# Performance work log

Hardware: AMD Instinct MI355X
Metric: run time of the kernel (lower is better)

## Reference

```python
import jax, jax.numpy as jnp
import numpy as np

N_NODES = 50000
N_EDGES = 800000
N_GRAPHS = 64
IN_DIM = 128
HID = 256
N_LAYERS = 4
N_PROT = 5
N_CLASSES = 1
EPS = 1e-12


def setup_inputs() -> dict:
    key = jax.random.key(0)
    ks = jax.random.split(key, 10)
    h = jax.random.normal(ks[0], (N_NODES, IN_DIM), jnp.float32)
    src = jax.random.randint(ks[1], (N_EDGES,), 0, N_NODES, dtype=jnp.int32)
    dst = jax.random.randint(ks[2], (N_EDGES,), 0, N_NODES, dtype=jnp.int32)
    graph_id = jnp.sort(jax.random.randint(ks[3], (N_NODES,), 0, N_GRAPHS, dtype=jnp.int32))
    W_emb = jax.random.normal(ks[4], (IN_DIM, HID), jnp.float32) * 0.05
    b_emb = jnp.zeros((HID,), jnp.float32)
    Ws = jax.random.normal(ks[5], (N_LAYERS, 2 * HID, HID), jnp.float32) * 0.05
    bs = jnp.zeros((N_LAYERS, HID), jnp.float32)
    p_pos = jax.random.uniform(ks[6], (N_PROT, HID), jnp.float32)
    p_neg = jax.random.uniform(ks[7], (N_PROT, HID), jnp.float32)
    W_fc = jax.random.normal(ks[8], (N_CLASSES, 2 * N_PROT), jnp.float32) * 0.1
    return dict(h=h, src=src, dst=dst, graph_id=graph_id, W_emb=W_emb,
                b_emb=b_emb, Ws=Ws, bs=bs, p_pos=p_pos, p_neg=p_neg, W_fc=W_fc)


def _segment_mean(x, seg, num):
    # sum over segments, divide by count (empty segments -> 0, like DGL mean)
    s = jax.ops.segment_sum(x, seg, num_segments=num)
    cnt = jax.ops.segment_sum(jnp.ones((x.shape[0],), x.dtype), seg, num_segments=num)
    return s / jnp.maximum(cnt, 1.0)[:, None]


def _forward(h, src, dst, graph_id, W_emb, b_emb, Ws, bs, p_pos, p_neg, W_fc):
    x = h @ W_emb + b_emb  # [N, HID]
    for l in range(N_LAYERS):
        # mean aggregation of neighbor messages (copy_src -> mean at dst)
        c = _segment_mean(x[src], dst, N_NODES)  # [N, HID]
        bundle = jnp.concatenate([x, c], axis=1) @ Ws[l] + bs[l]  # [N, HID]
        # F.normalize(p=2, dim=1) then relu activation, then residual add
        norm = jnp.linalg.norm(bundle, axis=1, keepdims=True)
        bundle = bundle / jnp.maximum(norm, EPS)
        x = x + jax.nn.relu(bundle)
    hg = _segment_mean(x, graph_id, N_GRAPHS)  # dgl.mean_nodes -> [G, HID]

    def sims(P):
        d = jnp.sum((hg[:, None, :] - P[None, :, :]) ** 2, axis=-1)  # [G, P]
        return jnp.log((d + 1.0) / (d + EPS))

    ss = jnp.concatenate([sims(p_pos), sims(p_neg)], axis=1)  # [G, 2P]
    y = ss @ W_fc.T  # [G, n_classes]
    return jax.nn.sigmoid(y).squeeze()


def reference(h, src, dst, graph_id, W_emb, b_emb, Ws, bs, p_pos, p_neg, W_fc):
    return _forward(h, src, dst, graph_id, W_emb, b_emb, Ws, bs, p_pos, p_neg, W_fc)
```

## Files before the change

### kernel.cpp

```cpp
#include <hip/hip_runtime.h>
#include <math.h>

#define N_NODESC 50000
#define NPAD 50048
#define N_EDGESC 800000
#define N_GRAPHSC 64
#define IN_DIMC 128
#define HIDC 256
#define N_LAYERSC 4
#define EPSV 1e-12f

#define NBUCK 196
#define EPB 4096
#define NBLK1 196
#define WCONV_BLKS 2176

typedef __attribute__((ext_vector_type(8))) short short8;
typedef __attribute__((ext_vector_type(4))) float floatx4;
typedef __attribute__((ext_vector_type(2))) float floatx2;

__device__ __forceinline__ unsigned short f2b(float f) {
    union { float f; unsigned u; } v; v.f = f;
    unsigned r = v.u + 0x7FFFu + ((v.u >> 16) & 1u);
    return (unsigned short)(r >> 16);
}
__device__ __forceinline__ unsigned pkb(float a, float b) {
    return (unsigned)f2b(a) | ((unsigned)f2b(b) << 16);
}
__device__ __forceinline__ unsigned char f2q(float v) {
    return (unsigned char)(__builtin_amdgcn_cvt_pk_fp8_f32(v, v, 0, false) & 0xFF);
}
__device__ __forceinline__ float q2f(unsigned u) {
    floatx2 t = __builtin_amdgcn_cvt_pk_f32_fp8(u, false);
    return t.x;
}
__device__ __forceinline__ unsigned pk4q(float a, float b, float c, float d) {
    unsigned lo = (unsigned)__builtin_amdgcn_cvt_pk_fp8_f32(a, b, 0, false) & 0xFFFFu;
    unsigned hi = (unsigned)__builtin_amdgcn_cvt_pk_fp8_f32(c, d, 0, false) << 16;
    return lo | hi;
}
__device__ __forceinline__ void ldscp16(const void* g, void* l) {
    __builtin_amdgcn_global_load_lds(
        (const __attribute__((address_space(1))) unsigned int*)g,
        (__attribute__((address_space(3))) unsigned int*)l, 16, 0, 0);
}

__global__ __launch_bounds__(256) void k_pre1(const float* __restrict__ Wemb,
        const float* __restrict__ Ws, unsigned short* __restrict__ wsw,
        unsigned char* __restrict__ wq, const int* __restrict__ gid,
        int* __restrict__ gstart, const int* __restrict__ dst,
        int* __restrict__ gbcnt) {
    __shared__ int bc[256];
    int b = blockIdx.x;
    int t = threadIdx.x;
    if (b < WCONV_BLKS) {
        int idx = b * 256 + t;
        const int EMB = IN_DIMC * HIDC;
        const int LYR = 2 * HIDC * HIDC;
        if (idx < EMB) {
            int k = idx >> 8, n = idx & 255;
            int off = (((k >> 5) * 16 + (n >> 4)) * 64 + ((((k >> 3) & 3) << 4) | (n & 15))) * 8 + (k & 7);
            wsw[off] = f2b(Wemb[idx]);
        } else if (idx < EMB + N_LAYERSC * LYR) {
            int r = idx - EMB;
            int l = r >> 17;
            int r2 = r & (LYR - 1);
            int k = r2 >> 8, n = r2 & 255;
            int off = (((k >> 5) * 16 + (n >> 4)) * 64 + ((((k >> 3) & 3) << 4) | (n & 15))) * 8 + (k & 7);
            wq[(size_t)l * LYR + off] = f2q(Ws[r]);
        }
    } else if (b == WCONV_BLKS) {
        int g = t;
        if (g <= N_GRAPHSC) {
            int lo = 0, hi = N_NODESC;
            while (lo < hi) {
                int mid = (lo + hi) >> 1;
                if (gid[mid] < g) lo = mid + 1; else hi = mid;
            }
            gstart[g] = lo;
        }
    } else {
        bc[t] = 0;
        __syncthreads();
        int e0 = (b - WCONV_BLKS - 1) * EPB;
        for (int i = t; i < EPB; i += 256) {
            int e = e0 + i;
            if (e < N_EDGESC) atomicAdd(&bc[dst[e] >> 8], 1);
        }
        __syncthreads();
        if (t < NBUCK && bc[t] > 0) atomicAdd(&gbcnt[t], bc[t]);
    }
}

__global__ __launch_bounds__(256) void k_bscan(const int* __restrict__ gbcnt,
        int* __restrict__ boffB, int* __restrict__ gcurB) {
    __shared__ int s[256];
    int t = threadIdx.x;
    int v = (t < NBUCK) ? gbcnt[t] : 0;
    s[t] = v;
    __syncthreads();
    for (int d = 1; d < 256; d <<= 1) {
        int u = (t >= d) ? s[t - d] : 0;
        __syncthreads();
        s[t] += u;
        __syncthreads();
    }
    if (t < NBUCK) {
        int excl = s[t] - v;
        boffB[t] = excl;
        gcurB[t] = excl;
    }
    if (t == 0) boffB[NBUCK] = N_EDGESC;
}

__global__ __launch_bounds__(256, 4) void k_scat_egemm(const int* __restrict__ src,
        const int* __restrict__ dst, int* __restrict__ gcurB,
        unsigned* __restrict__ ebpack, const float* __restrict__ h,
        const unsigned short* __restrict__ wsw, const float* __restrict__ bias,
        unsigned char* __restrict__ xq) {
    __shared__ int bc[256];
    __shared__ int cur[256];
    if (blockIdx.x < NBLK1) {
        int t = threadIdx.x;
        bc[t] = 0;
        __syncthreads();
        int e0 = blockIdx.x * EPB;
        for (int i = t; i < EPB; i += 256) {
            int e = e0 + i;
            if (e < N_EDGESC) atomicAdd(&bc[dst[e] >> 8], 1);
        }
        __syncthreads();
        if (t < NBUCK)
            cur[t] = (bc[t] > 0) ? atomicAdd(&gcurB[t], bc[t]) : 0;
        __syncthreads();
        for (int i = t; i < EPB; i += 256) {
            int e = e0 + i;
            if (e < N_EDGESC) {
                int d = dst[e];
                int b = d >> 8;
                int pos = atomicAdd(&cur[b], 1);
                ebpack[pos] = (unsigned)src[e] | ((unsigned)(d & 255) << 16);
            }
        }
        return;
    }
    int tid = threadIdx.x;
    int wn = tid >> 6;
    int lane = tid & 63;
    int quad = lane >> 4;
    int l15 = lane & 15;
    int row0 = (blockIdx.x - NBLK1) * 32;

    floatx4 acc[2][4];
    #pragma unroll
    for (int mt = 0; mt < 2; mt++)
        #pragma unroll
        for (int n = 0; n < 4; n++)
            acc[mt][n] = (floatx4){0.f, 0.f, 0.f, 0.f};

    int r0 = row0 + l15;
    int r1 = row0 + 16 + l15;
    bool ok0 = r0 < N_NODESC, ok1 = r1 < N_NODESC;
    const float* h0 = h + (size_t)r0 * IN_DIMC + quad * 8;
    const float* h1 = h + (size_t)r1 * IN_DIMC + quad * 8;
    const unsigned short* bp = wsw + ((size_t)(wn * 4) * 64 + lane) * 8;

    #pragma unroll
    for (int ks = 0; ks < 4; ks++) {
        float4 f00 = ok0 ? *(const float4*)(h0 + ks * 32)     : (float4){0,0,0,0};
        float4 f01 = ok0 ? *(const float4*)(h0 + ks * 32 + 4) : (float4){0,0,0,0};
        float4 f10 = ok1 ? *(const float4*)(h1 + ks * 32)     : (float4){0,0,0,0};
        float4 f11 = ok1 ? *(const float4*)(h1 + ks * 32 + 4) : (float4){0,0,0,0};
        short8 afr[2], bfr[4];
        uint4 av;
        av.x = pkb(f00.x, f00.y); av.y = pkb(f00.z, f00.w);
        av.z = pkb(f01.x, f01.y); av.w = pkb(f01.z, f01.w);
        afr[0] = *(short8*)&av;
        av.x = pkb(f10.x, f10.y); av.y = pkb(f10.z, f10.w);
        av.z = pkb(f11.x, f11.y); av.w = pkb(f11.z, f11.w);
        afr[1] = *(short8*)&av;
        const unsigned short* wp = bp + (size_t)ks * 8192;
        #pragma unroll
        for (int n = 0; n < 4; n++)
            bfr[n] = *(const short8*)(wp + n * 512);
        #pragma unroll
        for (int mt = 0; mt < 2; mt++)
            #pragma unroll
            for (int n = 0; n < 4; n++)
                acc[mt][n] = __builtin_amdgcn_mfma_f32_16x16x32_bf16(
                    afr[mt], bfr[n], acc[mt][n], 0, 0, 0);
    }

    float bv[4];
    #pragma unroll
    for (int n = 0; n < 4; n++) bv[n] = bias[wn * 64 + n * 16 + l15];
    #pragma unroll
    for (int mt = 0; mt < 2; mt++) {
        #pragma unroll
        for (int r = 0; r < 4; r++) {
            int row = row0 + mt * 16 + quad * 4 + r;
            if (row < N_NODESC) {
                #pragma unroll
                for (int n = 0; n < 4; n++) {
                    int col = wn * 64 + n * 16 + l15;
                    float v = acc[mt][n][r] + bv[n];
                    xq[(size_t)row * HIDC + col] = f2q(v);
                }
            }
        }
    }
}

__global__ __launch_bounds__(256) void k_bbuild(const unsigned* __restrict__ ebpack,
        const int* __restrict__ boffB, int* __restrict__ offs,
        unsigned short* __restrict__ esrc) {
    __shared__ int deg[256];
    __shared__ int lofs[256];
    __shared__ unsigned short img[12288];
    int b = blockIdx.x;
    int t = threadIdx.x;
    int bbase = boffB[b];
    int cnt = boffB[b + 1] - bbase;
    deg[t] = 0;
    __syncthreads();
    for (int i = t; i < cnt; i += 256)
        atomicAdd(&deg[ebpack[bbase + i] >> 16], 1);
    __syncthreads();
    int v = deg[t];
    lofs[t] = v;
    __syncthreads();
    for (int d = 1; d < 256; d <<= 1) {
        int u = (t >= d) ? lofs[t - d] : 0;
        __syncthreads();
        lofs[t] += u;
        __syncthreads();
    }
    int excl = lofs[t] - v;
    int node = b * 256 + t;
    if (node < N_NODESC) offs[node] = bbase + excl;
    if (b == NBUCK - 1 && t == 0) offs[N_NODESC] = N_EDGESC;
    deg[t] = excl;
    __syncthreads();
    for (int i = t; i < cnt; i += 256) {
        unsigned p = ebpack[bbase + i];
        int pos = atomicAdd(&deg[p >> 16], 1);
        img[pos] = (unsigned short)(p & 0xFFFF);
    }
    __syncthreads();
    for (int i = t; i < cnt; i += 256)
        esrc[bbase + i] = img[i];
}

__global__ __launch_bounds__(256, 8) void k_aggregate(const unsigned char* __restrict__ xq,
        const int* __restrict__ offs, const unsigned short* __restrict__ esrc,
        unsigned char* __restrict__ cq) {
    int gidx = blockIdx.x * 256 + threadIdx.x;
    int node = gidx >> 5;
    int lane = threadIdx.x & 31;
    if (node >= N_NODESC) return;
    int beg = offs[node], end = offs[node + 1];
    float a[8];
    #pragma unroll
    for (int j = 0; j < 8; j++) a[j] = 0.f;
    size_t loff = (size_t)lane * 8;
    int e = beg;
    #define ACC8(v) do { \
        floatx2 t0 = __builtin_amdgcn_cvt_pk_f32_fp8((v).x, false); \
        floatx2 t1 = __builtin_amdgcn_cvt_pk_f32_fp8((v).x, true);  \
        floatx2 t2 = __builtin_amdgcn_cvt_pk_f32_fp8((v).y, false); \
        floatx2 t3 = __builtin_amdgcn_cvt_pk_f32_fp8((v).y, true);  \
        a[0] += t0.x; a[1] += t0.y; a[2] += t1.x; a[3] += t1.y;     \
        a[4] += t2.x; a[5] += t2.y; a[6] += t3.x; a[7] += t3.y;     \
    } while (0)
    for (; e + 8 <= end; e += 8) {
        int sidx[8];
        #pragma unroll
        for (int j = 0; j < 8; j++) sidx[j] = esrc[e + j];
        uint2 v[8];
        #pragma unroll
        for (int j = 0; j < 8; j++)
            v[j] = *(const uint2*)(xq + (size_t)sidx[j] * HIDC + loff);
        #pragma unroll
        for (int j = 0; j < 8; j++) ACC8(v[j]);
    }
    if (e + 4 <= end) {
        int sidx[4];
        #pragma unroll
        for (int j = 0; j < 4; j++) sidx[j] = esrc[e + j];
        uint2 v[4];
        #pragma unroll
        for (int j = 0; j < 4; j++)
            v[j] = *(const uint2*)(xq + (size_t)sidx[j] * HIDC + loff);
        #pragma unroll
        for (int j = 0; j < 4; j++) ACC8(v[j]);
        e += 4;
    }
    for (; e < end; e++) {
        uint2 v = *(const uint2*)(xq + (size_t)esrc[e] * HIDC + loff);
        ACC8(v);
    }
    #undef ACC8
    float w = 1.0f / (float)max(end - beg, 1);
    uint2 o;
    o.x = pk4q(a[0] * w, a[1] * w, a[2] * w, a[3] * w);
    o.y = pk4q(a[4] * w, a[5] * w, a[6] * w, a[7] * w);
    *(uint2*)(cq + (size_t)node * HIDC + loff) = o;
}

template<bool LAST>
__global__ __launch_bounds__(256, 6) void k_lgemm(unsigned char* __restrict__ xq,
        const unsigned char* __restrict__ cq, const unsigned char* __restrict__ wq,
        const float* __restrict__ bias, const int* __restrict__ gid,
        float* __restrict__ hg) {
    __shared__ unsigned long long panelA64[1024];
    __shared__ unsigned long long panelC64[1024];
    __shared__ float rs[32];
    __shared__ signed char ggl[LAST ? 32 : 1];
    __shared__ int g0s;
    unsigned char* panelA = (unsigned char*)panelA64;
    unsigned char* panelC = (unsigned char*)panelC64;
    int tid = threadIdx.x;
    int w = tid >> 6;
    int lane = tid & 63;
    int quad = lane >> 4;
    int l15 = lane & 15;
    int row0 = blockIdx.x * 32;

    {
        int sboff = w * 2048 + lane * 16;
        #pragma unroll
        for (int i = 0; i < 2; i++) {
            int ldsoff = sboff + i * 1024;
            int r = ldsoff >> 8;
            int ch = (ldsoff & 255) >> 4;
            int lc = ch ^ (r & 15);
            ldscp16(xq + (size_t)(row0 + r) * HIDC + lc * 16, &panelA[w * 2048 + i * 1024]);
            ldscp16(cq + (size_t)(row0 + r) * HIDC + lc * 16, &panelC[w * 2048 + i * 1024]);
        }
    }
    __syncthreads();

    floatx4 acc[2][4];
    #pragma unroll
    for (int mt = 0; mt < 2; mt++)
        #pragma unroll
        for (int n = 0; n < 4; n++)
            acc[mt][n] = (floatx4){0.f, 0.f, 0.f, 0.f};

    const unsigned char* bp = wq + ((size_t)(w * 4) * 64 + lane) * 8;

    long long bcur[4], bnxt[4], acur[2], anxt[2];
    #pragma unroll
    for (int n = 0; n < 4; n++) bcur[n] = *(const long long*)(bp + n * 512);
    #pragma unroll
    for (int mt = 0; mt < 2; mt++) {
        int row = mt * 16 + l15;
        int lc = quad >> 1;
        int phys = lc ^ (row & 15);
        acur[mt] = *(const long long*)&panelA[row * 256 + phys * 16 + (quad & 1) * 8];
    }

    #pragma unroll
    for (int st = 0; st < 16; st++) {
        if (st < 15) {
            const unsigned char* wp = bp + (size_t)(st + 1) * 8192;
            #pragma unroll
            for (int n = 0; n < 4; n++)
                bnxt[n] = *(const long long*)(wp + n * 512);
            const unsigned char* pan2 = (st + 1 < 8) ? panelA : panelC;
            int ks2 = (st + 1) & 7;
            #pragma unroll
            for (int mt = 0; mt < 2; mt++) {
                int row = mt * 16 + l15;
                int lc = ks2 * 2 + (quad >> 1);
                int phys = lc ^ (row & 15);
                anxt[mt] = *(const long long*)&pan2[row * 256 + phys * 16 + (quad & 1) * 8];
            }
        }
        #pragma unroll
        for (int mt = 0; mt < 2; mt++)
            #pragma unroll
            for (int n = 0; n < 4; n++)
                acc[mt][n] = __builtin_amdgcn_mfma_f32_16x16x32_fp8_fp8(
                    acur[mt], bcur[n], acc[mt][n], 0, 0, 0);
        #pragma unroll
        for (int n = 0; n < 4; n++) bcur[n] = bnxt[n];
        #pragma unroll
        for (int mt = 0; mt < 2; mt++) acur[mt] = anxt[mt];
    }

    float bv[4];
    #pragma unroll
    for (int n = 0; n < 4; n++) bv[n] = bias[w * 64 + n * 16 + l15];
    #pragma unroll
    for (int mt = 0; mt < 2; mt++)
        #pragma unroll
        for (int n = 0; n < 4; n++)
            #pragma unroll
            for (int r = 0; r < 4; r++)
                acc[mt][n][r] += bv[n];

    __syncthreads();
    if (tid < 32) rs[tid] = 0.f;
    if constexpr (LAST) {
        if (tid < 32) {
            int g0 = gid[min(row0, N_NODESC - 1)];
            int gv = gid[min(row0 + tid, N_NODESC - 1)] - g0;
            ggl[tid] = (signed char)min(gv, 3);
            if (tid == 0) g0s = g0;
        }
    }
    __syncthreads();
    #pragma unroll
    for (int mt = 0; mt < 2; mt++) {
        #pragma unroll
        for (int r = 0; r < 4; r++) {
            float p = acc[mt][0][r] * acc[mt][0][r] + acc[mt][1][r] * acc[mt][1][r]
                    + acc[mt][2][r] * acc[mt][2][r] + acc[mt][3][r] * acc[mt][3][r];
            p += __shfl_xor(p, 1);
            p += __shfl_xor(p, 2);
            p += __shfl_xor(p, 4);
            p += __shfl_xor(p, 8);
            if (l15 == 0) atomicAdd(&rs[mt * 16 + quad * 4 + r], p);
        }
    }
    __syncthreads();

    #pragma unroll
    for (int mt = 0; mt < 2; mt++) {
        #pragma unroll
        for (int r = 0; r < 4; r++) {
            int lrow = mt * 16 + quad * 4 + r;
            int row = row0 + lrow;
            float inv = 1.0f / fmaxf(sqrtf(rs[mt * 16 + quad * 4 + r]), EPSV);
            #pragma unroll
            for (int n = 0; n < 4; n++) {
                int phys = (w * 4 + n) ^ (lrow & 15);
                float xo = q2f((unsigned)panelA[lrow * 256 + phys * 16 + l15]);
                float nv = xo + fmaxf(acc[mt][n][r] * inv, 0.f);
                if constexpr (LAST) {
                    acc[mt][n][r] = nv;
                } else if (row < N_NODESC) {
                    int col = w * 64 + n * 16 + l15;
                    xq[(size_t)row * HIDC + col] = f2q(nv);
                }
            }
        }
    }
    if constexpr (LAST) {
        int nspan = (int)ggl[31] + 1;
        int g0 = g0s;
        for (int gl = 0; gl < nspan; gl++) {
            float s[4] = {0.f, 0.f, 0.f, 0.f};
            #pragma unroll
            for (int mt = 0; mt < 2; mt++) {
                #pragma unroll
                for (int r = 0; r < 4; r++) {
                    int lrow = mt * 16 + quad * 4 + r;
                    bool m = ((int)ggl[lrow] == gl) && (row0 + lrow < N_NODESC);
                    float f = m ? 1.f : 0.f;
                    #pragma unroll
                    for (int n = 0; n < 4; n++) s[n] += f * acc[mt][n][r];
                }
            }
            #pragma unroll
            for (int n = 0; n < 4; n++) {
                s[n] += __shfl_xor(s[n], 16);
                s[n] += __shfl_xor(s[n], 32);
            }
            if (quad == 0) {
                #pragma unroll
                for (int n = 0; n < 4; n++)
                    atomicAdd(&hg[(g0 + gl) * HIDC + w * 64 + n * 16 + l15], s[n]);
            }
        }
    }
}

__global__ __launch_bounds__(256) void k_readout(const float* __restrict__ hg,
        const int* __restrict__ gstart, const float* __restrict__ ppos,
        const float* __restrict__ pneg, const float* __restrict__ wfc,
        float* __restrict__ out) {
    __shared__ float red[256];
    __shared__ float ss[10];
    int t = threadIdx.x;
    int g = blockIdx.x;
    int beg = gstart[g], end = gstart[g + 1];
    float inv = 1.0f / (float)max(end - beg, 1);
    float hgv = hg[g * HIDC + t] * inv;
    for (int p = 0; p < 10; p++) {
        const float* P = (p < 5) ? (ppos + p * HIDC) : (pneg + (p - 5) * HIDC);
        float d = hgv - P[t];
        red[t] = d * d;
        __syncthreads();
        for (int s2 = 128; s2 > 0; s2 >>= 1) {
            if (t < s2) red[t] += red[t + s2];
            __syncthreads();
        }
        if (t == 0) {
            float dd = red[0];
            ss[p] = logf((dd + 1.0f) / (dd + EPSV));
        }
        __syncthreads();
    }
    if (t == 0) {
        float y = 0.f;
        #pragma unroll
        for (int p = 0; p < 10; p++) y += ss[p] * wfc[p];
        out[g] = 1.0f / (1.0f + expf(-y));
    }
}

extern "C" void kernel_launch(void* const* d_in, const int* in_sizes, int n_in,
                              void* d_out, int out_size, void* d_ws, size_t ws_size,
                              hipStream_t stream) {
    const float* h    = (const float*)d_in[0];
    const int*   src  = (const int*)d_in[1];
    const int*   dst  = (const int*)d_in[2];
    const int*   gid  = (const int*)d_in[3];
    const float* Wemb = (const float*)d_in[4];
    const float* bemb = (const float*)d_in[5];
    const float* Ws   = (const float*)d_in[6];
    const float* bs   = (const float*)d_in[7];
    const float* ppos = (const float*)d_in[8];
    const float* pneg = (const float*)d_in[9];
    const float* wfc  = (const float*)d_in[10];
    float* out = (float*)d_out;

    char* ws = (char*)d_ws;
    size_t off = 0;
    auto alloc = [&](size_t bytes) {
        void* p = ws + off;
        off += (bytes + 255) & ~(size_t)255;
        return p;
    };
    unsigned char*  xq     = (unsigned char*)alloc((size_t)NPAD * HIDC);
    unsigned char*  cq     = (unsigned char*)alloc((size_t)NPAD * HIDC);
    unsigned short* wsw    = (unsigned short*)alloc((size_t)(IN_DIMC * HIDC) * 2);
    unsigned char*  wq     = (unsigned char*)alloc((size_t)(N_LAYERSC * 2 * HIDC * HIDC));
    int*            offs   = (int*)alloc((size_t)(N_NODESC + 1) * 4);
    unsigned short* esrc   = (unsigned short*)alloc((size_t)N_EDGESC * 2);
    unsigned*       ebpack = (unsigned*)alloc((size_t)N_EDGESC * 4);
    int*            gbcnt  = (int*)alloc((size_t)NBUCK * 4);
    int*            boffB  = (int*)alloc((size_t)(NBUCK + 1) * 4);
    int*            gcurB  = (int*)alloc((size_t)NBUCK * 4);
    int*            gstart = (int*)alloc((size_t)(N_GRAPHSC + 1) * 4);
    float*          hg     = (float*)alloc((size_t)N_GRAPHSC * HIDC * 4);
    (void)ws_size; (void)in_sizes; (void)n_in; (void)out_size;

    hipMemsetAsync(gbcnt, 0, (size_t)NBUCK * 4, stream);
    hipMemsetAsync(hg, 0, (size_t)N_GRAPHSC * HIDC * 4, stream);

    const int LYR = 2 * HIDC * HIDC;
    k_pre1<<<WCONV_BLKS + 1 + NBLK1, 256, 0, stream>>>(Wemb, Ws, wsw, wq, gid, gstart, dst, gbcnt);
    k_bscan<<<1, 256, 0, stream>>>(gbcnt, boffB, gcurB);
    k_scat_egemm<<<NBLK1 + NPAD / 32, 256, 0, stream>>>(src, dst, gcurB, ebpack, h, wsw, bemb, xq);
    k_bbuild<<<NBUCK, 256, 0, stream>>>(ebpack, boffB, offs, esrc);

    for (int l = 0; l < N_LAYERSC; l++) {
        k_aggregate<<<(N_NODESC * 32 + 255) / 256, 256, 0, stream>>>(xq, offs, esrc, cq);
        if (l < N_LAYERSC - 1)
            k_lgemm<false><<<NPAD / 32, 256, 0, stream>>>(
                xq, cq, wq + (size_t)l * LYR, bs + (size_t)l * HIDC, gid, hg);
        else
            k_lgemm<true><<<NPAD / 32, 256, 0, stream>>>(
                xq, cq, wq + (size_t)l * LYR, bs + (size_t)l * HIDC, gid, hg);
    }
    k_readout<<<N_GRAPHSC, 256, 0, stream>>>(hg, gstart, ppos, pneg, wfc, out);
}
```

Before: 368.3 us.

## Pad per-node edge lists to multiples of eight and widen aggregate gathers

The CSR build now pads each node's neighbour list to a multiple of eight entries, filling the padding with a sentinel that points at a zeroed pad row of the feature matrix. Each bucket gets a fixed 8192-slot region, and a separate per-node degree array holds the true count used for the mean. The aggregation kernel drops its remainder loops and uses 16 lanes per node with 16-byte feature loads and vectorised index loads prefetched one group ahead, aiming for fewer, wider memory transactions and less control overhead. In exchange it issues extra gathers of the zero row, and it relies on the pad row staying zero and on each padded bucket fitting in 8192 slots.

```diff
diff --git a/kernel.cpp b/kernel.cpp
--- a/kernel.cpp
+++ b/kernel.cpp
@@ -14,6 +14,8 @@
 #define EPB 4096
 #define NBLK1 196
 #define WCONV_BLKS 2176
+#define PBUCK 8192
+#define ZROW 50000
 
 typedef __attribute__((ext_vector_type(8))) short short8;
 typedef __attribute__((ext_vector_type(4))) float floatx4;
@@ -199,13 +201,11 @@
         #pragma unroll
         for (int r = 0; r < 4; r++) {
             int row = row0 + mt * 16 + quad * 4 + r;
-            if (row < N_NODESC) {
-                #pragma unroll
-                for (int n = 0; n < 4; n++) {
-                    int col = wn * 64 + n * 16 + l15;
-                    float v = acc[mt][n][r] + bv[n];
-                    xq[(size_t)row * HIDC + col] = f2q(v);
-                }
+            #pragma unroll
+            for (int n = 0; n < 4; n++) {
+                int col = wn * 64 + n * 16 + l15;
+                float v = acc[mt][n][r] + bv[n];
+                xq[(size_t)row * HIDC + col] = (row < N_NODESC) ? f2q(v) : (unsigned char)0;
             }
         }
     }
@@ -213,10 +213,10 @@
 
 __global__ __launch_bounds__(256) void k_bbuild(const unsigned* __restrict__ ebpack,
         const int* __restrict__ boffB, int* __restrict__ offs,
-        unsigned short* __restrict__ esrc) {
+        int* __restrict__ ndeg, unsigned short* __restrict__ esrc) {
     __shared__ int deg[256];
     __shared__ int lofs[256];
-    __shared__ unsigned short img[12288];
+    __shared__ unsigned short img[PBUCK];
     int b = blockIdx.x;
     int t = threadIdx.x;
     int bbase = boffB[b];
@@ -226,20 +226,26 @@
     for (int i = t; i < cnt; i += 256)
         atomicAdd(&deg[ebpack[bbase + i] >> 16], 1);
     __syncthreads();
-    int v = deg[t];
-    lofs[t] = v;
-    __syncthreads();
-    for (int d = 1; d < 256; d <<= 1) {
-        int u = (t >= d) ? lofs[t - d] : 0;
+    int d = deg[t];
+    int pd = (d + 7) & ~7;
+    lofs[t] = pd;
+    __syncthreads();
+    for (int s = 1; s < 256; s <<= 1) {
+        int u = (t >= s) ? lofs[t - s] : 0;
         __syncthreads();
         lofs[t] += u;
         __syncthreads();
     }
-    int excl = lofs[t] - v;
+    int pexcl = lofs[t] - pd;
     int node = b * 256 + t;
-    if (node < N_NODESC) offs[node] = bbase + excl;
-    if (b == NBUCK - 1 && t == 0) offs[N_NODESC] = N_EDGESC;
-    deg[t] = excl;
+    int S = b * PBUCK;
+    if (node < N_NODESC) {
+        offs[node] = S + pexcl;
+        ndeg[node] = d;
+    }
+    int ptot = lofs[255];
+    for (int i = t; i < ptot; i += 256) img[i] = (unsigned short)ZROW;
+    deg[t] = pexcl;
     __syncthreads();
     for (int i = t; i < cnt; i += 256) {
         unsigned p = ebpack[bbase + i];
@@ -247,64 +253,60 @@
         img[pos] = (unsigned short)(p & 0xFFFF);
     }
     __syncthreads();
-    for (int i = t; i < cnt; i += 256)
-        esrc[bbase + i] = img[i];
-}
-
-__global__ __launch_bounds__(256, 8) void k_aggregate(const unsigned char* __restrict__ xq,
-        const int* __restrict__ offs, const unsigned short* __restrict__ esrc,
-        unsigned char* __restrict__ cq) {
+    for (int i = t; i < ptot; i += 256)
+        esrc[S + i] = img[i];
+}
+
+__global__ __launch_bounds__(256, 6) void k_aggregate(const unsigned char* __restrict__ xq,
+        const int* __restrict__ offs, const int* __restrict__ ndeg,
+        const unsigned short* __restrict__ esrc, unsigned char* __restrict__ cq) {
     int gidx = blockIdx.x * 256 + threadIdx.x;
-    int node = gidx >> 5;
-    int lane = threadIdx.x & 31;
-    if (node >= N_NODESC) return;
-    int beg = offs[node], end = offs[node + 1];
-    float a[8];
-    #pragma unroll
-    for (int j = 0; j < 8; j++) a[j] = 0.f;
-    size_t loff = (size_t)lane * 8;
-    int e = beg;
-    #define ACC8(v) do { \
-        floatx2 t0 = __builtin_amdgcn_cvt_pk_f32_fp8((v).x, false); \
-        floatx2 t1 = __builtin_amdgcn_cvt_pk_f32_fp8((v).x, true);  \
-        floatx2 t2 = __builtin_amdgcn_cvt_pk_f32_fp8((v).y, false); \
-        floatx2 t3 = __builtin_amdgcn_cvt_pk_f32_fp8((v).y, true);  \
-        a[0] += t0.x; a[1] += t0.y; a[2] += t1.x; a[3] += t1.y;     \
-        a[4] += t2.x; a[5] += t2.y; a[6] += t3.x; a[7] += t3.y;     \
+    int node = gidx >> 4;
+    int lane = threadIdx.x & 15;
+    int beg = offs[node];
+    int dn = ndeg[node];
+    int pd = (dn + 7) & ~7;
+    int end = beg + pd;
+    float a[16];
+    #pragma unroll
+    for (int j = 0; j < 16; j++) a[j] = 0.f;
+    size_t loff = (size_t)lane * 16;
+
+    #define C4(u, o) do { \
+        floatx2 t0 = __builtin_amdgcn_cvt_pk_f32_fp8((u), false); \
+        floatx2 t1 = __builtin_amdgcn_cvt_pk_f32_fp8((u), true);  \
+        a[(o)] += t0.x; a[(o)+1] += t0.y; a[(o)+2] += t1.x; a[(o)+3] += t1.y; \
     } while (0)
-    for (; e + 8 <= end; e += 8) {
-        int sidx[8];
-        #pragma unroll
-        for (int j = 0; j < 8; j++) sidx[j] = esrc[e + j];
-        uint2 v[8];
-        #pragma unroll
-        for (int j = 0; j < 8; j++)
-            v[j] = *(const uint2*)(xq + (size_t)sidx[j] * HIDC + loff);
-        #pragma unroll
-        for (int j = 0; j < 8; j++) ACC8(v[j]);
-    }
-    if (e + 4 <= end) {
-        int sidx[4];
-        #pragma unroll
-        for (int j = 0; j < 4; j++) sidx[j] = esrc[e + j];
-        uint2 v[4];
-        #pragma unroll
-        for (int j = 0; j < 4; j++)
-            v[j] = *(const uint2*)(xq + (size_t)sidx[j] * HIDC + loff);
-        #pragma unroll
-        for (int j = 0; j < 4; j++) ACC8(v[j]);
-        e += 4;
-    }
-    for (; e < end; e++) {
-        uint2 v = *(const uint2*)(xq + (size_t)esrc[e] * HIDC + loff);
-        ACC8(v);
-    }
-    #undef ACC8
-    float w = 1.0f / (float)max(end - beg, 1);
-    uint2 o;
-    o.x = pk4q(a[0] * w, a[1] * w, a[2] * w, a[3] * w);
-    o.y = pk4q(a[4] * w, a[5] * w, a[6] * w, a[7] * w);
-    *(uint2*)(cq + (size_t)node * HIDC + loff) = o;
+
+    if (pd > 0) {
+        uint4 si = *(const uint4*)&esrc[beg];
+        for (int e = beg; e < end; e += 8) {
+            uint4 sin;
+            if (e + 8 < end) sin = *(const uint4*)&esrc[e + 8];
+            int ix[8];
+            ix[0] = si.x & 0xFFFF; ix[1] = si.x >> 16;
+            ix[2] = si.y & 0xFFFF; ix[3] = si.y >> 16;
+            ix[4] = si.z & 0xFFFF; ix[5] = si.z >> 16;
+            ix[6] = si.w & 0xFFFF; ix[7] = si.w >> 16;
+            uint4 v[8];
+            #pragma unroll
+            for (int j = 0; j < 8; j++)
+                v[j] = *(const uint4*)(xq + (size_t)ix[j] * HIDC + loff);
+            #pragma unroll
+            for (int j = 0; j < 8; j++) {
+                C4(v[j].x, 0); C4(v[j].y, 4); C4(v[j].z, 8); C4(v[j].w, 12);
+            }
+            si = sin;
+        }
+    }
+    #undef C4
+    float w = 1.0f / (float)max(dn, 1);
+    uint4 o;
+    o.x = pk4q(a[0] * w,  a[1] * w,  a[2] * w,  a[3] * w);
+    o.y = pk4q(a[4] * w,  a[5] * w,  a[6] * w,  a[7] * w);
+    o.z = pk4q(a[8] * w,  a[9] * w,  a[10] * w, a[11] * w);
+    o.w = pk4q(a[12] * w, a[13] * w, a[14] * w, a[15] * w);
+    *(uint4*)(cq + (size_t)node * HIDC + loff) = o;
 }
 
 template<bool LAST>
@@ -539,7 +541,8 @@
     unsigned short* wsw    = (unsigned short*)alloc((size_t)(IN_DIMC * HIDC) * 2);
     unsigned char*  wq     = (unsigned char*)alloc((size_t)(N_LAYERSC * 2 * HIDC * HIDC));
     int*            offs   = (int*)alloc((size_t)(N_NODESC + 1) * 4);
-    unsigned short* esrc   = (unsigned short*)alloc((size_t)N_EDGESC * 2);
+    int*            ndeg   = (int*)alloc((size_t)N_NODESC * 4);
+    unsigned short* esrc   = (unsigned short*)alloc((size_t)NBUCK * PBUCK * 2);
     unsigned*       ebpack = (unsigned*)alloc((size_t)N_EDGESC * 4);
     int*            gbcnt  = (int*)alloc((size_t)NBUCK * 4);
     int*            boffB  = (int*)alloc((size_t)(NBUCK + 1) * 4);
@@ -555,10 +558,10 @@
     k_pre1<<<WCONV_BLKS + 1 + NBLK1, 256, 0, stream>>>(Wemb, Ws, wsw, wq, gid, gstart, dst, gbcnt);
     k_bscan<<<1, 256, 0, stream>>>(gbcnt, boffB, gcurB);
     k_scat_egemm<<<NBLK1 + NPAD / 32, 256, 0, stream>>>(src, dst, gcurB, ebpack, h, wsw, bemb, xq);
-    k_bbuild<<<NBUCK, 256, 0, stream>>>(ebpack, boffB, offs, esrc);
+    k_bbuild<<<NBUCK, 256, 0, stream>>>(ebpack, boffB, offs, ndeg, esrc);
 
     for (int l = 0; l < N_LAYERSC; l++) {
-        k_aggregate<<<(N_NODESC * 32 + 255) / 256, 256, 0, stream>>>(xq, offs, esrc, cq);
+        k_aggregate<<<(N_NODESC * 16 + 255) / 256, 256, 0, stream>>>(xq, offs, ndeg, esrc, cq);
         if (l < N_LAYERSC - 1)
             k_lgemm<false><<<NPAD / 32, 256, 0, stream>>>(
                 xq, cq, wq + (size_t)l * LYR, bs + (size_t)l * HIDC, gid, hg);
```

After: 1.174 ms. 219% more time.
